# Performance work log

Measured on AMD Instinct MI355X. Metric: run time of the kernel, lower is better.

The kernel has to match this reference:

```python
import jax, jax.numpy as jnp
import numpy as np

F = 8          # number of fields (field 0 is a sequence field)
V = 100000     # vocab per field
D = 16         # latent_dim
B = 4096       # batch
L = 50         # sequence length for field 0


def setup_inputs() -> dict:
    key = jax.random.key(0)
    k1, k2, k3, k4, k5, k6 = jax.random.split(key, 6)
    x_seq = jax.random.randint(k1, (B, L), 0, V, dtype=jnp.int32)
    x_cat = jax.random.randint(k2, (B, F - 1), 0, V, dtype=jnp.int32)
    # field-aware tables: ffm_tables[i, j] is the embedding table of field i used against field j
    ffm_tables = jax.random.normal(k3, (F, F, V, D), dtype=jnp.float32) * 0.01
    # linear (1-dim) embedding table per field
    lin_tables = jax.random.normal(k4, (F, V), dtype=jnp.float32) * 0.01
    dense_w = jax.random.normal(k5, (F, 1), dtype=jnp.float32) * 0.1
    dense_b = jnp.zeros((1,), dtype=jnp.float32)
    return {"x_seq": x_seq, "x_cat": x_cat, "ffm_tables": ffm_tables,
            "lin_tables": lin_tables, "dense_w": dense_w, "dense_b": dense_b}


def reference(x_seq, x_cat, ffm_tables, lin_tables, dense_w, dense_b):
    # pooled[i] has shape [F, B, D]: embedding of field i under each of its F target tables
    pooled = [ffm_tables[0][:, x_seq].mean(axis=2)]  # sequence field: [F,B,L,D] -> mean over L
    for f in range(1, F):
        pooled.append(ffm_tables[f][:, x_cat[:, f - 1]])  # [F,B,D]
    P = jnp.stack(pooled)  # [F, F, B, D]; P[i, j] = emb of field i with table i->j

    ii, jj = np.triu_indices(F, k=1)  # all pairs i<j (28 pairs)
    # sum over pairs of dot(e_{i->j}(x_i), e_{j->i}(x_j))
    ffm = jnp.einsum('pbd,pbd->b', P[ii, jj], P[jj, ii])  # [B]

    # linear term: per-field 1-dim embeddings (mean-pooled for sequence), then Dense(1, relu)
    lin0 = lin_tables[0][x_seq].mean(axis=1)  # [B]
    lin_rest = lin_tables[1:][np.arange(F - 1)[:, None], x_cat.T]  # [F-1, B]
    Z = jnp.concatenate([lin0[None], lin_rest], axis=0).T  # [B, F]
    lin = jax.nn.relu(Z @ dense_w + dense_b)  # [B, 1]

    # broadcast add ([B,1,1] matches tf.add of [B,1] linear and [B,1,1] fm term)
    out = jax.nn.sigmoid(lin[:, :, None] + ffm[:, None, None])  # [B, 1, 1]
    return out
```

## Files before the change

### kernel.cpp

```cpp
#include <hip/hip_runtime.h>

namespace {

constexpr int kF = 8;
constexpr int kV = 100000;
constexpr int kD = 16;
constexpr int kL = 50;
constexpr int kNC = 7;
constexpr int kNP = 21;

__constant__ unsigned char cPI[kNP] = {1,1,1,1,1,1,2,2,2,2,2,3,3,3,3,4,4,4,5,5,6};
__constant__ unsigned char cPJ[kNP] = {2,3,4,5,6,7,3,4,5,6,7,4,5,6,7,5,6,7,6,7,7};

__global__ __launch_bounds__(256) void ffm_fwd(
    const int* __restrict__ xs,
    const int* __restrict__ xc,
    const float* __restrict__ T,
    const float* __restrict__ Lt,
    const float* __restrict__ dw,
    const float* __restrict__ db,
    float* __restrict__ out)
{
    const int b = blockIdx.x;
    const int tid = threadIdx.x;

    __shared__ int sidx[kL];
    __shared__ int cat[kNC];
    __shared__ float w0[kNC][kD];
    __shared__ float r1[4], r2[4];

    if (tid < kL) sidx[tid] = xs[b * kL + tid];
    if (tid >= 64 && tid < 64 + kNC) cat[tid - 64] = xc[b * kNC + (tid - 64)];
    __syncthreads();

    float facc = 0.f;
    float sacc = 0.f;
    float zacc = 0.f;

    if (tid < kNC * 4) {
        const int j = tid >> 2, q = tid & 3;
        const float4 v = *(const float4*)(
            T + ((size_t)((j + 1) * kF + 0) * kV + cat[j]) * kD + q * 4);
        *(float4*)(&w0[j][q * 4]) = v;
    }
    {
        const int t = tid - 32;
        if (t >= 0 && t < kNP * 4) {
            const int p = t >> 2, q = t & 3;
            const int i = cPI[p], j = cPJ[p];
            const float4 a = *(const float4*)(
                T + ((size_t)(i * kF + j) * kV + cat[i - 1]) * kD + q * 4);
            const float4 c = *(const float4*)(
                T + ((size_t)(j * kF + i) * kV + cat[j - 1]) * kD + q * 4);
            facc += a.x * c.x + a.y * c.y + a.z * c.z + a.w * c.w;
        }
    }
    if (tid >= 128 && tid < 128 + kL) {
        zacc += Lt[sidx[tid - 128]] * dw[0] * (1.0f / kL);
    }
    if (tid >= 192 && tid < 192 + kNC) {
        const int f = tid - 192 + 1;
        zacc += Lt[(size_t)f * kV + cat[f - 1]] * dw[f];
    }
    __syncthreads();

    if (tid < 224) {
        const int q = tid & 3;
        const int j = (tid >> 2) % kNC;
        const int l0 = tid / 28;
        const float4 w = *(const float4*)(&w0[j][q * 4]);
        const float* base = T + (size_t)(j + 1) * kV * kD + q * 4;
        for (int l = l0; l < kL; l += 8) {
            const float4 a = *(const float4*)(base + (size_t)sidx[l] * kD);
            sacc += a.x * w.x + a.y * w.y + a.z * w.z + a.w * w.w;
        }
    }

    float v1 = facc + sacc * (1.0f / kL);
    float v2 = zacc;
    #pragma unroll
    for (int o = 32; o > 0; o >>= 1) {
        v1 += __shfl_xor(v1, o, 64);
        v2 += __shfl_xor(v2, o, 64);
    }
    const int wave = tid >> 6;
    if ((tid & 63) == 0) { r1[wave] = v1; r2[wave] = v2; }
    __syncthreads();
    if (tid == 0) {
        const float ffm_sum = r1[0] + r1[1] + r1[2] + r1[3];
        float z = r2[0] + r2[1] + r2[2] + r2[3] + db[0];
        z = fmaxf(z, 0.f);
        const float x = z + ffm_sum;
        out[b] = 1.f / (1.f + expf(-x));
    }
}

}

extern "C" void kernel_launch(void* const* d_in, const int* in_sizes, int n_in,
                              void* d_out, int out_size, void* d_ws, size_t ws_size,
                              hipStream_t stream) {
    const int* xs = (const int*)d_in[0];
    const int* xc = (const int*)d_in[1];
    const float* T = (const float*)d_in[2];
    const float* Lt = (const float*)d_in[3];
    const float* dw = (const float*)d_in[4];
    const float* db = (const float*)d_in[5];
    float* out = (float*)d_out;
    const int B = in_sizes[0] / kL;
    hipLaunchKernelGGL(ffm_fwd, dim3(B), dim3(256), 0, stream,
                       xs, xc, T, Lt, dw, db, out);
}
```

Before: 474.1 us.

## Stage all categorical embeddings in shared memory and flatten sequence gather loop

Each block now loads every categorical field's embedding row against all target tables into shared memory in a single wide phase, then computes the pairwise dot products from shared memory. The sequence-field gather is flattened so all 256 threads cover the 50x7x4 work items in an unrolled loop. The aim is to issue more independent loads at once so that gather latency overlaps, instead of running serial dependent loops on 224 threads. The cost is more shared memory per block and some extra integer div/mod work for index computation.

```diff
diff --git a/kernel.cpp b/kernel.cpp
--- a/kernel.cpp
+++ b/kernel.cpp
@@ -26,54 +26,52 @@
 
     __shared__ int sidx[kL];
     __shared__ int cat[kNC];
-    __shared__ float w0[kNC][kD];
+    __shared__ float sE[kNC][kF][kD];
     __shared__ float r1[4], r2[4];
 
     if (tid < kL) sidx[tid] = xs[b * kL + tid];
-    if (tid >= 64 && tid < 64 + kNC) cat[tid - 64] = xc[b * kNC + (tid - 64)];
+    else if (tid >= 64 && tid < 64 + kNC) cat[tid - 64] = xc[b * kNC + (tid - 64)];
     __syncthreads();
 
     float facc = 0.f;
     float sacc = 0.f;
     float zacc = 0.f;
 
-    if (tid < kNC * 4) {
-        const int j = tid >> 2, q = tid & 3;
+    if (tid < 196) {
+        const int p = tid >> 2, q = tid & 3;
+        const int i = 1 + p / 7;
+        const int jj = p % 7;
+        const int j = jj + (jj >= i);
         const float4 v = *(const float4*)(
-            T + ((size_t)((j + 1) * kF + 0) * kV + cat[j]) * kD + q * 4);
-        *(float4*)(&w0[j][q * 4]) = v;
-    }
-    {
-        const int t = tid - 32;
-        if (t >= 0 && t < kNP * 4) {
-            const int p = t >> 2, q = t & 3;
-            const int i = cPI[p], j = cPJ[p];
-            const float4 a = *(const float4*)(
-                T + ((size_t)(i * kF + j) * kV + cat[i - 1]) * kD + q * 4);
-            const float4 c = *(const float4*)(
-                T + ((size_t)(j * kF + i) * kV + cat[j - 1]) * kD + q * 4);
-            facc += a.x * c.x + a.y * c.y + a.z * c.z + a.w * c.w;
-        }
-    }
-    if (tid >= 128 && tid < 128 + kL) {
-        zacc += Lt[sidx[tid - 128]] * dw[0] * (1.0f / kL);
-    }
-    if (tid >= 192 && tid < 192 + kNC) {
-        const int f = tid - 192 + 1;
-        zacc += Lt[(size_t)f * kV + cat[f - 1]] * dw[f];
+            T + ((size_t)(i * kF + j) * kV + cat[i - 1]) * kD + q * 4);
+        *(float4*)(&sE[i - 1][j][q * 4]) = v;
+    } else if (tid < 246) {
+        zacc = Lt[sidx[tid - 196]] * dw[0] * (1.0f / kL);
+    } else if (tid < 253) {
+        const int f = tid - 246 + 1;
+        zacc = Lt[(size_t)f * kV + cat[f - 1]] * dw[f];
     }
     __syncthreads();
 
-    if (tid < 224) {
-        const int q = tid & 3;
-        const int j = (tid >> 2) % kNC;
-        const int l0 = tid / 28;
-        const float4 w = *(const float4*)(&w0[j][q * 4]);
-        const float* base = T + (size_t)(j + 1) * kV * kD + q * 4;
-        for (int l = l0; l < kL; l += 8) {
-            const float4 a = *(const float4*)(base + (size_t)sidx[l] * kD);
+    #pragma unroll
+    for (int k = 0; k < 6; ++k) {
+        const int t = tid + 256 * k;
+        if (t < kL * kNC * 4) {
+            const int l = t / 28, r = t % 28;
+            const int jf = (r >> 2) + 1, q = r & 3;
+            const float4 a = *(const float4*)(
+                T + ((size_t)jf * kV + (size_t)sidx[l]) * kD + q * 4);
+            const float4 w = *(const float4*)(&sE[jf - 1][0][q * 4]);
             sacc += a.x * w.x + a.y * w.y + a.z * w.z + a.w * w.w;
         }
+    }
+
+    if (tid >= 128 && tid < 128 + kNP * 4) {
+        const int p = (tid - 128) >> 2, q = (tid - 128) & 3;
+        const int i = cPI[p], j = cPJ[p];
+        const float* A = &sE[i - 1][j][q * 4];
+        const float* C = &sE[j - 1][i][q * 4];
+        facc = A[0] * C[0] + A[1] * C[1] + A[2] * C[2] + A[3] * C[3];
     }
 
     float v1 = facc + sacc * (1.0f / kL);
```

Result: no change. 476.2 us (+0.4%).
